# Kernel tuning notes

Hardware: AMD Instinct MI355X
Metric: run time of the kernel (lower is better)

Reference implementation:

```python
import jax, jax.numpy as jnp
import numpy as np

PRED_WEIGHT = 1.0
GT_WEIGHT = 1.0
EPS = 1e-9
P = 16384
G = 16384


def setup_inputs() -> dict:
    key = jax.random.key(0)
    k1, k2, k3, k4 = jax.random.split(key, 4)
    return {
        "pred_points": jax.random.normal(k1, (P, 3), dtype=jnp.float32),
        "gt_points": jax.random.normal(k2, (G, 3), dtype=jnp.float32),
        "w_pred": jax.random.uniform(k3, (P,), dtype=jnp.float32),
        "w_gt": jax.random.uniform(k4, (G,), dtype=jnp.float32),
    }


def reference(pred_points, gt_points, w_pred, w_gt):
    # squared pairwise distances: ||p||^2 + ||g||^2 - 2 p.g, clamped at 0
    p2 = jnp.sum(pred_points * pred_points, axis=1)  # (P,)
    g2 = jnp.sum(gt_points * gt_points, axis=1)      # (G,)
    d2 = p2[:, None] + g2[None, :] - 2.0 * (pred_points @ gt_points.T)  # (P, G)
    d2 = jnp.maximum(d2, 0.0)
    min_pred = jnp.min(d2, axis=1)  # (P,)
    min_gt = jnp.min(d2, axis=0)    # (G,)
    weighted_pred = jnp.sum(w_pred * min_pred) / jnp.maximum(jnp.sum(w_pred), EPS)
    weighted_gt = jnp.sum(w_gt * min_gt) / jnp.maximum(jnp.sum(w_gt), EPS)
    return PRED_WEIGHT * weighted_pred + GT_WEIGHT * weighted_gt
```

## Files before the change

kernel.cpp:

```cpp
#include <hip/hip_runtime.h>
#include <math.h>


constexpr int NPTS  = 16384;
constexpr int BLOCK = 512;
constexpr int WAVES = BLOCK / 64;

constexpr int ROWS_PER_BLOCK = 512;
constexpr int COLS_PER_BLOCK = 512;
constexpr int NBX = NPTS / ROWS_PER_BLOCK;
constexpr int NBY = NPTS / COLS_PER_BLOCK;
constexpr int NBLOCKS = NBX * NBY * 2;
constexpr int ROWS_PER_WAVE = ROWS_PER_BLOCK / WAVES;
constexpr int CSTEPS = COLS_PER_BLOCK / 64;

typedef __attribute__((ext_vector_type(8)))  __bf16 bf16x8;
typedef __attribute__((ext_vector_type(16))) float  f32x16;

__device__ inline unsigned short f2bf(float f) {
    unsigned u = __float_as_uint(f);
    u += 0x7FFFu + ((u >> 16) & 1u);
    return (unsigned short)(u >> 16);
}
__device__ inline float bf2f(unsigned short h) {
    return __uint_as_float(((unsigned)h) << 16);
}
__device__ inline unsigned pk(unsigned short lo, unsigned short hi) {
    return (unsigned)lo | ((unsigned)hi << 16);
}

__global__ __launch_bounds__(256) void pack_init_kernel(
    const float* __restrict__ pred, const float* __restrict__ gt,
    uint4* __restrict__ Af, uint4* __restrict__ Bf,
    uint4* __restrict__ Ag, uint4* __restrict__ Bp,
    unsigned int* __restrict__ minP, unsigned int* __restrict__ minG,
    unsigned int* __restrict__ ticket)
{
    const unsigned short ONE = 0x3F80;
    int i = blockIdx.x * 256 + threadIdx.x;
    if (i == 0) *ticket = 0u;
    if (i >= NPTS) return;

    {
        float x = pred[3*i], y = pred[3*i+1], z = pred[3*i+2];
        unsigned short hx = f2bf(x), hy = f2bf(y), hz = f2bf(z);
        unsigned short lx = f2bf(x - bf2f(hx));
        unsigned short ly = f2bf(y - bf2f(hy));
        unsigned short lz = f2bf(z - bf2f(hz));
        float p2 = fmaf(x, x, fmaf(y, y, z * z));
        unsigned short sh = f2bf(p2), sl = f2bf(p2 - bf2f(sh));
        uint4 a0, a1, b0, b1;
        a0.x = pk(hx, hy); a0.y = pk(hz, lx); a0.z = pk(ly, lz); a0.w = pk(hx, hy);
        a1.x = pk(hz, sh); a1.y = pk(sl, ONE); a1.z = pk(ONE, lx); a1.w = pk(ly, lz);
        b0.x = pk(hx, hy); b0.y = pk(hz, hx); b0.z = pk(hy, hz); b0.w = pk(lx, ly);
        b1.x = pk(lz, ONE); b1.y = pk(ONE, sh); b1.z = pk(sl, lx); b1.w = pk(ly, lz);
        Af[i] = a0; Af[NPTS + i] = a1;
        Bp[i] = b0; Bp[NPTS + i] = b1;
    }
    {
        float gx = gt[3*i], gy = gt[3*i+1], gz = gt[3*i+2];
        float mx = -2.0f * gx, my = -2.0f * gy, mz = -2.0f * gz;
        unsigned short hx = f2bf(mx), hy = f2bf(my), hz = f2bf(mz);
        unsigned short lx = f2bf(mx - bf2f(hx));
        unsigned short ly = f2bf(my - bf2f(hy));
        unsigned short lz = f2bf(mz - bf2f(hz));
        float g2 = fmaf(gx, gx, fmaf(gy, gy, gz * gz));
        unsigned short sh = f2bf(g2), sl = f2bf(g2 - bf2f(sh));
        uint4 a0, a1, b0, b1;
        a0.x = pk(hx, hy); a0.y = pk(hz, lx); a0.z = pk(ly, lz); a0.w = pk(hx, hy);
        a1.x = pk(hz, sh); a1.y = pk(sl, ONE); a1.z = pk(ONE, lx); a1.w = pk(ly, lz);
        b0.x = pk(hx, hy); b0.y = pk(hz, hx); b0.z = pk(hy, hz); b0.w = pk(lx, ly);
        b1.x = pk(lz, ONE); b1.y = pk(ONE, sh); b1.z = pk(sl, lx); b1.w = pk(ly, lz);
        Ag[i] = a0; Ag[NPTS + i] = a1;
        Bf[i] = b0; Bf[NPTS + i] = b1;
    }
    minP[i] = 0x7F800000u;
    minG[i] = 0x7F800000u;
}

__device__ inline float tree32(const f32x16 a, const f32x16 b) {
    float m0 = fminf(fminf(a[0],  a[1]),  a[2]);
    float m1 = fminf(fminf(a[3],  a[4]),  a[5]);
    float m2 = fminf(fminf(a[6],  a[7]),  a[8]);
    float m3 = fminf(fminf(a[9],  a[10]), a[11]);
    float m4 = fminf(fminf(a[12], a[13]), a[14]);
    float m5 = fminf(fminf(a[15], b[0]),  b[1]);
    float m6 = fminf(fminf(b[2],  b[3]),  b[4]);
    float m7 = fminf(fminf(b[5],  b[6]),  b[7]);
    float m8 = fminf(fminf(b[8],  b[9]),  b[10]);
    float m9 = fminf(fminf(b[11], b[12]), b[13]);
    float ma = fminf(b[14], b[15]);
    float n0 = fminf(fminf(m0, m1), m2);
    float n1 = fminf(fminf(m3, m4), m5);
    float n2 = fminf(fminf(m6, m7), m8);
    float n3 = fminf(fminf(m9, ma), n0);
    return fminf(fminf(n1, n2), n3);
}

__global__ __launch_bounds__(BLOCK, 2) void chamfer_mfma_kernel(
    const uint4* __restrict__ Af, const uint4* __restrict__ Bf,
    const uint4* __restrict__ Ag, const uint4* __restrict__ Bp,
    unsigned int* __restrict__ minP, unsigned int* __restrict__ minG,
    const float* __restrict__ wpred, const float* __restrict__ wgt,
    unsigned int* __restrict__ ticket, float* __restrict__ out)
{
    const int tid  = threadIdx.x;
    const int wv   = tid >> 6;
    const int lane = tid & 63;
    const int half = lane >> 5;
    const int ln31 = lane & 31;

    const uint4* __restrict__ Aside;
    const uint4* __restrict__ Bside;
    unsigned int* __restrict__ outMin;
    if (blockIdx.z == 0) { Aside = Af; Bside = Bf; outMin = minG; }
    else                 { Aside = Ag; Bside = Bp; outMin = minP; }

    const int rowBase = blockIdx.x * ROWS_PER_BLOCK + wv * ROWS_PER_WAVE;
    const int colBase = blockIdx.y * COLS_PER_BLOCK;

    __shared__ uint4 sBf[2 * COLS_PER_BLOCK];
    __shared__ unsigned int cminS[COLS_PER_BLOCK];

    #pragma unroll
    for (int p = 0; p < (2 * COLS_PER_BLOCK) / BLOCK; ++p) {
        int idx = p * BLOCK + tid;
        int h = idx >> 9;
        int c = idx & (COLS_PER_BLOCK - 1);
        sBf[idx] = Bside[h * NPTS + colBase + c];
    }
    for (int c = tid; c < COLS_PER_BLOCK; c += BLOCK)
        cminS[c] = 0x7F800000u;
    __syncthreads();

    const uint4* __restrict__ Ah = Aside + half * NPTS;
    const uint4* sB = sBf + half * COLS_PER_BLOCK;

    bf16x8 af0 = __builtin_bit_cast(bf16x8, Ah[rowBase + ln31]);
    bf16x8 af1 = __builtin_bit_cast(bf16x8, Ah[rowBase + 32 + ln31]);

    const f32x16 zacc = {0.f,0.f,0.f,0.f, 0.f,0.f,0.f,0.f,
                         0.f,0.f,0.f,0.f, 0.f,0.f,0.f,0.f};

    #pragma unroll 2
    for (int s = 0; s < CSTEPS; ++s) {
        bf16x8 b0 = __builtin_bit_cast(bf16x8, sB[s * 64 + ln31]);
        bf16x8 b1 = __builtin_bit_cast(bf16x8, sB[s * 64 + 32 + ln31]);
        f32x16 p0 = __builtin_amdgcn_mfma_f32_32x32x16_bf16(af0, b0, zacc, 0, 0, 0);
        f32x16 q0 = __builtin_amdgcn_mfma_f32_32x32x16_bf16(af1, b0, zacc, 0, 0, 0);
        f32x16 p1 = __builtin_amdgcn_mfma_f32_32x32x16_bf16(af0, b1, zacc, 0, 0, 0);
        f32x16 q1 = __builtin_amdgcn_mfma_f32_32x32x16_bf16(af1, b1, zacc, 0, 0, 0);
        float c0 = fmaxf(tree32(p0, q0), 0.0f);
        float c1 = fmaxf(tree32(p1, q1), 0.0f);
        atomicMin(&cminS[s * 64 + ln31],      __float_as_uint(c0));
        atomicMin(&cminS[s * 64 + 32 + ln31], __float_as_uint(c1));
    }

    __syncthreads();
    for (int c = tid; c < COLS_PER_BLOCK; c += BLOCK)
        atomicMin(&outMin[colBase + c], cminS[c]);

    __shared__ unsigned int sTicket;
    asm volatile("s_waitcnt vmcnt(0)" ::: "memory");
    __syncthreads();
    if (tid == 0) sTicket = atomicAdd(ticket, 1u);
    __syncthreads();
    if (sTicket != (unsigned)(NBLOCKS - 1)) return;

    float np = 0.f, dp = 0.f, ng = 0.f, dg = 0.f;
    for (int i = tid; i < NPTS; i += BLOCK) {
        float v = __uint_as_float(atomicMin(&minP[i], 0xFFFFFFFFu));
        float w = wpred[i];
        np = fmaf(w, v, np); dp += w;
        float u = __uint_as_float(atomicMin(&minG[i], 0xFFFFFFFFu));
        float x = wgt[i];
        ng = fmaf(x, u, ng); dg += x;
    }
    #pragma unroll
    for (int off = 1; off < 64; off <<= 1) {
        np += __shfl_xor(np, off, 64);
        dp += __shfl_xor(dp, off, 64);
        ng += __shfl_xor(ng, off, 64);
        dg += __shfl_xor(dg, off, 64);
    }
    __shared__ float sred[4][WAVES];
    if (lane == 0) { sred[0][wv] = np; sred[1][wv] = dp;
                     sred[2][wv] = ng; sred[3][wv] = dg; }
    __syncthreads();
    if (tid == 0) {
        float NP = 0.f, DP = 0.f, NG = 0.f, DG = 0.f;
        #pragma unroll
        for (int k = 0; k < WAVES; ++k) {
            NP += sred[0][k]; DP += sred[1][k];
            NG += sred[2][k]; DG += sred[3][k];
        }
        out[0] = NP / fmaxf(DP, 1e-9f) + NG / fmaxf(DG, 1e-9f);
    }
}

extern "C" void kernel_launch(void* const* d_in, const int* in_sizes, int n_in,
                              void* d_out, int out_size, void* d_ws, size_t ws_size,
                              hipStream_t stream)
{
    const float* pred  = (const float*)d_in[0];
    const float* gt    = (const float*)d_in[1];
    const float* wpred = (const float*)d_in[2];
    const float* wgt   = (const float*)d_in[3];
    float* out = (float*)d_out;

    uint4* Af = (uint4*)d_ws;
    uint4* Bf = Af + 2 * NPTS;
    uint4* Ag = Bf + 2 * NPTS;
    uint4* Bp = Ag + 2 * NPTS;
    unsigned int* minP = (unsigned int*)(Bp + 2 * NPTS);
    unsigned int* minG = minP + NPTS;
    unsigned int* ticket = minG + NPTS;

    pack_init_kernel<<<NPTS / 256, 256, 0, stream>>>(
        pred, gt, Af, Bf, Ag, Bp, minP, minG, ticket);

    chamfer_mfma_kernel<<<dim3(NBX, NBY, 2), BLOCK, 0, stream>>>(
        Af, Bf, Ag, Bp, minP, minG, wpred, wgt, ticket, out);
}
```

Measured before the change: 98.81 us.

## Widen column tile to 1024 and move final reduction to separate kernel

Doubles the columns each block handles, which halves the grid and the number of global atomicMin flushes per row-block pair while doubling shared-memory staging. Replaces the last-block ticket scheme, with its per-block vmcnt wait, global atomicAdd and atomic reads, by a separate single-block 1024-thread finalize kernel that does plain loads. This removes the ticket serialization from every block but adds another kernel launch, and the larger tile reduces the number of blocks available to fill the GPU.

```diff
diff --git a/kernel.cpp b/kernel.cpp
--- a/kernel.cpp
+++ b/kernel.cpp
@@ -7,10 +7,9 @@
 constexpr int WAVES = BLOCK / 64;
 
 constexpr int ROWS_PER_BLOCK = 512;
-constexpr int COLS_PER_BLOCK = 512;
+constexpr int COLS_PER_BLOCK = 1024;
 constexpr int NBX = NPTS / ROWS_PER_BLOCK;
 constexpr int NBY = NPTS / COLS_PER_BLOCK;
-constexpr int NBLOCKS = NBX * NBY * 2;
 constexpr int ROWS_PER_WAVE = ROWS_PER_BLOCK / WAVES;
 constexpr int CSTEPS = COLS_PER_BLOCK / 64;
 
@@ -33,12 +32,10 @@
     const float* __restrict__ pred, const float* __restrict__ gt,
     uint4* __restrict__ Af, uint4* __restrict__ Bf,
     uint4* __restrict__ Ag, uint4* __restrict__ Bp,
-    unsigned int* __restrict__ minP, unsigned int* __restrict__ minG,
-    unsigned int* __restrict__ ticket)
+    unsigned int* __restrict__ minP, unsigned int* __restrict__ minG)
 {
     const unsigned short ONE = 0x3F80;
     int i = blockIdx.x * 256 + threadIdx.x;
-    if (i == 0) *ticket = 0u;
     if (i >= NPTS) return;
 
     {
@@ -100,13 +97,11 @@
 __global__ __launch_bounds__(BLOCK, 2) void chamfer_mfma_kernel(
     const uint4* __restrict__ Af, const uint4* __restrict__ Bf,
     const uint4* __restrict__ Ag, const uint4* __restrict__ Bp,
-    unsigned int* __restrict__ minP, unsigned int* __restrict__ minG,
-    const float* __restrict__ wpred, const float* __restrict__ wgt,
-    unsigned int* __restrict__ ticket, float* __restrict__ out)
+    unsigned int* __restrict__ minP, unsigned int* __restrict__ minG)
 {
     const int tid  = threadIdx.x;
+    const int lane = tid & 63;
     const int wv   = tid >> 6;
-    const int lane = tid & 63;
     const int half = lane >> 5;
     const int ln31 = lane & 31;
 
@@ -125,7 +120,7 @@
     #pragma unroll
     for (int p = 0; p < (2 * COLS_PER_BLOCK) / BLOCK; ++p) {
         int idx = p * BLOCK + tid;
-        int h = idx >> 9;
+        int h = idx >> 10;
         int c = idx & (COLS_PER_BLOCK - 1);
         sBf[idx] = Bside[h * NPTS + colBase + c];
     }
@@ -157,22 +152,30 @@
     }
 
     __syncthreads();
-    for (int c = tid; c < COLS_PER_BLOCK; c += BLOCK)
+    #pragma unroll
+    for (int p = 0; p < COLS_PER_BLOCK / BLOCK; ++p) {
+        int c = p * BLOCK + tid;
         atomicMin(&outMin[colBase + c], cminS[c]);
-
-    __shared__ unsigned int sTicket;
-    asm volatile("s_waitcnt vmcnt(0)" ::: "memory");
-    __syncthreads();
-    if (tid == 0) sTicket = atomicAdd(ticket, 1u);
-    __syncthreads();
-    if (sTicket != (unsigned)(NBLOCKS - 1)) return;
+    }
+}
+
+__global__ __launch_bounds__(1024) void finalize_kernel(
+    const unsigned int* __restrict__ minP,
+    const unsigned int* __restrict__ minG,
+    const float* __restrict__ wpred, const float* __restrict__ wgt,
+    float* __restrict__ out)
+{
+    const int tid  = threadIdx.x;
+    const int lane = tid & 63;
+    const int wv   = tid >> 6;
 
     float np = 0.f, dp = 0.f, ng = 0.f, dg = 0.f;
-    for (int i = tid; i < NPTS; i += BLOCK) {
-        float v = __uint_as_float(atomicMin(&minP[i], 0xFFFFFFFFu));
+    #pragma unroll 4
+    for (int i = tid; i < NPTS; i += 1024) {
+        float v = __uint_as_float(minP[i]);
         float w = wpred[i];
         np = fmaf(w, v, np); dp += w;
-        float u = __uint_as_float(atomicMin(&minG[i], 0xFFFFFFFFu));
+        float u = __uint_as_float(minG[i]);
         float x = wgt[i];
         ng = fmaf(x, u, ng); dg += x;
     }
@@ -183,14 +186,14 @@
         ng += __shfl_xor(ng, off, 64);
         dg += __shfl_xor(dg, off, 64);
     }
-    __shared__ float sred[4][WAVES];
+    __shared__ float sred[4][16];
     if (lane == 0) { sred[0][wv] = np; sred[1][wv] = dp;
                      sred[2][wv] = ng; sred[3][wv] = dg; }
     __syncthreads();
     if (tid == 0) {
         float NP = 0.f, DP = 0.f, NG = 0.f, DG = 0.f;
         #pragma unroll
-        for (int k = 0; k < WAVES; ++k) {
+        for (int k = 0; k < 16; ++k) {
             NP += sred[0][k]; DP += sred[1][k];
             NG += sred[2][k]; DG += sred[3][k];
         }
@@ -214,11 +217,12 @@
     uint4* Bp = Ag + 2 * NPTS;
     unsigned int* minP = (unsigned int*)(Bp + 2 * NPTS);
     unsigned int* minG = minP + NPTS;
-    unsigned int* ticket = minG + NPTS;
 
     pack_init_kernel<<<NPTS / 256, 256, 0, stream>>>(
-        pred, gt, Af, Bf, Ag, Bp, minP, minG, ticket);
+        pred, gt, Af, Bf, Ag, Bp, minP, minG);
 
     chamfer_mfma_kernel<<<dim3(NBX, NBY, 2), BLOCK, 0, stream>>>(
-        Af, Bf, Ag, Bp, minP, minG, wpred, wgt, ticket, out);
-}
+        Af, Bf, Ag, Bp, minP, minG);
+
+    finalize_kernel<<<1, 1024, 0, stream>>>(minP, minG, wpred, wgt, out);
+}
```

After: 83.42 us. 1.18x faster.
